# Kernel tuning notes

Hardware: AMD Instinct MI355X
Metric: run time of the kernel (lower is better)

## Reference

```python
import jax, jax.numpy as jnp
import numpy as np

# ---- static problem config (matches init_kwargs / input_specs) ----
L = 8                      # num_labels
D = H = W = 96             # volume dims
N = D * H * W
ALPHA, BETA, GAMMA = 8.0, 0.125, 3.0
NIT = 5                    # num_iterations
# 4-D bilateral grid dims: 3 spatial axes scaled by alpha, 1 intensity axis scaled by beta
GD = (int(np.ceil((D - 1) / ALPHA)) + 2,
      int(np.ceil((H - 1) / ALPHA)) + 2,
      int(np.ceil((W - 1) / ALPHA)) + 2,
      int(np.ceil(1.0 / BETA)) + 2)
GSIZE = int(np.prod(GD))
_STRIDES = np.array([GD[1] * GD[2] * GD[3], GD[2] * GD[3], GD[3], 1], dtype=np.int32)


def spatial_gaussian(Q):
    """Exact separable 3D Gaussian filter with sigma=GAMMA. Q: (L, D, H, W)."""
    r = int(3 * GAMMA)
    t = jnp.arange(-r, r + 1, dtype=Q.dtype)
    k = jnp.exp(-0.5 * (t / GAMMA) ** 2)
    k = k / k.sum()
    x = Q[None]  # (1, L, D, H, W)
    for ax in range(3):
        kspatial = [1, 1, 1]
        kspatial[ax] = 2 * r + 1
        kern = jnp.broadcast_to(k.reshape([1, 1] + kspatial), [L, 1] + kspatial)
        pad = [(r, r) if i == ax else (0, 0) for i in range(3)]
        x = jax.lax.conv_general_dilated(
            x, kern, (1, 1, 1), pad, feature_group_count=L,
            dimension_numbers=('NCDHW', 'OIDHW', 'NCDHW'))
    return x[0]


def splat_coords(img):
    """4-D lattice features per voxel. img: (D, H, W). Returns lo (4,N) int32, frac (4,N)."""
    zz, yy, xx = jnp.meshgrid(jnp.arange(D, dtype=img.dtype),
                              jnp.arange(H, dtype=img.dtype),
                              jnp.arange(W, dtype=img.dtype), indexing='ij')
    feats = jnp.stack([zz.reshape(-1) / ALPHA,
                       yy.reshape(-1) / ALPHA,
                       xx.reshape(-1) / ALPHA,
                       img.reshape(-1) / BETA], axis=0)  # (4, N)
    hi = jnp.asarray(GD, feats.dtype).reshape(4, 1) - 2.0
    lo_f = jnp.clip(jnp.floor(feats), 0.0, hi)
    frac = feats - lo_f
    return lo_f.astype(jnp.int32), frac


def blur1(g, ax):
    """[1,2,1]/4 blur along axis ax (grid-unit Gaussian of the splat-blur-slice)."""
    pad = [(0, 0)] * g.ndim
    pad[ax] = (1, 1)
    gp = jnp.pad(g, pad)
    n = g.shape[ax]
    a = jax.lax.slice_in_dim(gp, 0, n, axis=ax)
    b = jax.lax.slice_in_dim(gp, 1, n + 1, axis=ax)
    c = jax.lax.slice_in_dim(gp, 2, n + 2, axis=ax)
    return 0.25 * a + 0.5 * b + 0.25 * c


def lattice_filter(vals, lo, frac):
    """Splat-blur-slice high-dim Gaussian filter. vals: (C, N) -> (C, N)."""
    C = vals.shape[0]
    grid = jnp.zeros((C, GSIZE), vals.dtype)
    idxs, ws = [], []
    for bits in range(16):  # 16 corners of the 4-D cell (multilinear splat)
        off = np.array([(bits >> d) & 1 for d in range(4)], dtype=np.int32)
        w = jnp.prod(jnp.where(off[:, None] == 1, frac, 1.0 - frac), axis=0)  # (N,)
        idx = jnp.sum((lo + off[:, None]) * _STRIDES[:, None], axis=0)        # (N,)
        idxs.append(idx)
        ws.append(w)
        grid = grid.at[:, idx].add(vals * w[None])
    g = grid.reshape((C,) + GD)
    for ax in range(1, 5):
        g = blur1(g, ax)
    gf = g.reshape(C, GSIZE)
    out = jnp.zeros_like(vals)
    for bits in range(16):  # slice
        out = out + ws[bits][None] * gf[:, idxs[bits]]
    return out


def bilateral_apply(Q, lo, frac):
    """Normalized bilateral filtering of Q (L, D, H, W)."""
    vals = jnp.concatenate([Q.reshape(L, N), jnp.ones((1, N), Q.dtype)], axis=0)
    out = lattice_filter(vals, lo, frac)
    return (out[:L] / (out[L:] + 1e-8)).reshape(L, D, H, W)


def reference(U, image, spatial_ker_weights, bilateral_ker_weights, compatibility_matrix):
    Us = U[0]                               # (L, D, H, W); batch must be 1
    lo, frac = splat_coords(image[0, 0])    # lattice built once from image (as in __init__)
    Q = Us
    for _ in range(NIT):
        # NOTE: original code recomputes softmax of the (unchanged) unary U each iteration
        Qsm = jax.nn.softmax(Us, axis=0)
        sp = spatial_gaussian(Qsm).reshape(L, -1)
        bi = bilateral_apply(Qsm, lo, frac).reshape(L, -1)
        Qp = compatibility_matrix @ (spatial_ker_weights @ sp + bilateral_ker_weights @ bi)
        Q = Us + Qp.reshape(L, D, H, W)
    return jax.nn.softmax(Q, axis=0)[None]


def setup_inputs() -> dict:
    key = jax.random.key(0)
    k1, k2 = jax.random.split(key)
    U = jax.random.normal(k1, (1, L, D, H, W), jnp.float32)
    image = jax.random.uniform(k2, (1, 1, D, H, W), jnp.float32)
    eye = jnp.eye(L, dtype=jnp.float32)
    return {
        "U": U,
        "image": image,
        "spatial_ker_weights": 3.0 * eye,     # spatial_ker_weight * I
        "bilateral_ker_weights": 10.0 * eye,  # bilateral_ker_weight * I
        "compatibility_matrix": eye,
    }
```

## Files before the change

kernel.cpp:

```cpp
#include <hip/hip_runtime.h>
#include <math.h>

#define LBL   8
#define DIM   96
#define PLANE (DIM*DIM)
#define NVOX  (DIM*DIM*DIM)
#define GD0 14
#define GD1 14
#define GD2 14
#define GD3 10
#define GSIZE (GD0*GD1*GD2*GD3)
#define ST0 1960
#define ST1 140
#define ST2 10
#define CH  12
#define NBLK 12
#define NBLKS (NBLK*NBLK*NBLK)
#define PART 720
#define GOUT (GSIZE*9)
#define SUP 513
#define ROW8 (DIM/8)
#define PLANE8 (PLANE/8)
#define VOL8 (NVOX/8)
#define XY_BLOCKS 768
#define BLUR_BLOCKS ((GOUT + 255)/256)
#define GRIDF4 (GSIZE*CH/4)

typedef _Float16 half8 __attribute__((ext_vector_type(8)));

__device__ inline half8 h8zero() {
    half8 v;
    #pragma unroll
    for (int e = 0; e < 8; ++e) v[e] = (_Float16)0.f;
    return v;
}

__constant__ float GW[10] = {
    0.13317604f, 0.12597912f, 0.10663904f, 0.08077540f, 0.05475300f,
    0.03320771f, 0.01802341f, 0.00875346f, 0.00380423f, 0.00147945f
};

__global__ __launch_bounds__(512)
void k_zero(float4* __restrict__ g)
{
    const int i = blockIdx.x*512 + threadIdx.x;
    if (i < GRIDF4) {
        float4 z; z.x = 0.f; z.y = 0.f; z.z = 0.f; z.w = 0.f;
        g[i] = z;
    }
}

__global__ __launch_bounds__(512)
void k_softmax_splat(const float* __restrict__ U, const float* __restrict__ img,
                     _Float16* __restrict__ lnq, float* __restrict__ grid)
{
    __shared__ float sF[512];
    __shared__ __align__(16) unsigned char uball[2880 * 4];
    __shared__ _Float16 sA[64*180];

    _Float16* sU = (_Float16*)uball;
    float*    sB = (float*)uball;

    const int tid = threadIdx.x;
    const int bid0 = blockIdx.x;
    const int bid = (bid0 & 7) * (NBLKS >> 3) + (bid0 >> 3);
    const int bx = bid % NBLK;
    const int by = (bid / NBLK) % NBLK;
    const int bz = bid / (NBLK*NBLK);

    const int lx = tid & 7;
    const int ly = (tid >> 3) & 7;
    const int lz = tid >> 6;

    const int x = bx*8 + lx;
    const int y = by*8 + ly;
    const int z = bz*8 + lz;
    const int vox = z * PLANE + y * DIM + x;

    {
        float t[LBL], e[LBL];
        float m = -1e30f;
        #pragma unroll
        for (int l = 0; l < LBL; ++l) { t[l] = U[l*NVOX + vox]; m = fmaxf(m, t[l]); }
        float ssum = 0.f;
        #pragma unroll
        for (int l = 0; l < LBL; ++l) { t[l] -= m; e[l] = __expf(t[l]); ssum += e[l]; }
        const float inv  = 1.f / ssum;
        const float logs = __logf(ssum);
        #pragma unroll
        for (int l = 0; l < LBL; ++l) {
            lnq[l*NVOX + vox] = (_Float16)(t[l] - logs);
            sU[l*SUP + tid]   = (_Float16)(e[l] * inv);
        }
        sU[8*SUP + tid] = (_Float16)1.0f;
        sF[tid] = img[vox] * 8.0f;
    }
    __syncthreads();

    {
        const int cgrp = tid & 3;
        const int k2   = (tid >> 2) & 1;
        const int row  = tid >> 3;
        const int cb   = cgrp * 2;

        float bins[10][3];
        #pragma unroll
        for (int g = 0; g < 10; ++g) { bins[g][0]=0.f; bins[g][1]=0.f; bins[g][2]=0.f; }

        for (int vx = 0; vx < 8; ++vx) {
            const int vi = row*8 + vx;
            const float f  = sF[vi];
            const float wx = k2 ? (float)vx*0.125f : 1.f - (float)vx*0.125f;
            const float u0 = (float)sU[cb*SUP + vi];
            const float u1 = (float)sU[(cb+1)*SUP + vi];
            const float u2 = (float)sU[8*SUP + vi];
            #pragma unroll
            for (int g = 0; g < 10; ++g) {
                float w = fmaxf(1.f - fabsf(f - (float)g), 0.f) * wx;
                bins[g][0] += w*u0; bins[g][1] += w*u1; bins[g][2] += w*u2;
            }
        }
        _Float16* pA = sA + row*180 + k2*90;
        #pragma unroll
        for (int g = 0; g < 10; ++g) {
            pA[g*9 + cb]     = (_Float16)bins[g][0];
            pA[g*9 + cb + 1] = (_Float16)bins[g][1];
            if (cgrp == 3) pA[g*9 + 8] = (_Float16)bins[g][2];
        }
    }
    __syncthreads();

    if (tid < 288) {
        const int c   = tid % 9;
        const int k2  = (tid / 9) & 1;
        const int j2  = (tid / 18) & 1;
        const int lzo = tid / 36;
        float S[10];
        #pragma unroll
        for (int g = 0; g < 10; ++g) S[g] = 0.f;
        for (int ly2 = 0; ly2 < 8; ++ly2) {
            const float wy = j2 ? (float)ly2*0.125f : 1.f - (float)ly2*0.125f;
            const _Float16* pA = sA + (lzo*8 + ly2)*180 + k2*90;
            #pragma unroll
            for (int g = 0; g < 10; ++g) S[g] += wy * (float)pA[g*9 + c];
        }
        float* pB = sB + lzo*360 + j2*180 + k2*90;
        #pragma unroll
        for (int g = 0; g < 10; ++g) pB[g*9 + c] = S[g];
    }
    __syncthreads();

    for (int item = tid; item < PART; item += 512) {
        const int t  = item / 90;
        const int gc = item % 90;
        const int g  = gc / 9;
        const int c  = gc % 9;
        const int i2 = t >> 2, j2 = (t >> 1) & 1, k2 = t & 1;
        float acc = 0.f;
        #pragma unroll
        for (int lzo = 0; lzo < 8; ++lzo) {
            const float wz = i2 ? (float)lzo*0.125f : 1.f - (float)lzo*0.125f;
            acc += wz * sB[lzo*360 + j2*180 + k2*90 + gc];
        }
        const int cell = (bz + i2)*ST0 + (by + j2)*ST1 + (bx + k2)*ST2 + g;
        atomicAdd(&grid[cell*CH + c], acc);
    }
}

__global__ __launch_bounds__(256)
void k_xy_blur(const half8* __restrict__ lnq, half8* __restrict__ dst,
               const float* __restrict__ gsrc, float* __restrict__ gdst)
{
    __shared__ _Float16 sIn[PLANE];
    __shared__ _Float16 sX[PLANE];

    const int tid = threadIdx.x;

    if (blockIdx.x >= XY_BLOCKS) {
        const int item = (blockIdx.x - XY_BLOCKS)*256 + tid;
        if (item >= GOUT) return;
        const int c    = item % 9;
        const int cell = item / 9;
        const int gz = cell / ST0;
        int r = cell % ST0;
        const int gy = r / ST1;  r %= ST1;
        const int gx = r / ST2;
        const int g  = r % ST2;

        const int crd[4] = {gz, gy, gx, g};
        const int ext[4] = {GD0, GD1, GD2, GD3};
        const int str[4] = {ST0, ST1, ST2, 1};
        float wa[4][3];
        int   oa[4][3];
        #pragma unroll
        for (int ax = 0; ax < 4; ++ax)
            #pragma unroll
            for (int dd = 0; dd < 3; ++dd) {
                const int cc = crd[ax] + dd - 1;
                const bool ok = (cc >= 0 && cc < ext[ax]);
                wa[ax][dd] = ok ? (dd == 1 ? 0.5f : 0.25f) : 0.f;
                oa[ax][dd] = ok ? (dd - 1) * str[ax] : 0;
            }

        float acc = 0.f;
        #pragma unroll
        for (int a = 0; a < 3; ++a) {
            const float w0 = wa[0][a];
            #pragma unroll
            for (int b = 0; b < 3; ++b) {
                const float w1 = w0 * wa[1][b];
                #pragma unroll
                for (int d2 = 0; d2 < 3; ++d2) {
                    const float w2 = w1 * wa[2][d2];
                    const int ob = oa[0][a] + oa[1][b] + oa[2][d2];
                    #pragma unroll
                    for (int e = 0; e < 3; ++e)
                        acc += w2 * wa[3][e] * gsrc[(cell + ob + oa[3][e])*CH + c];
                }
            }
        }
        gdst[cell*CH + c] = acc;
        return;
    }

    half8* sIn8 = (half8*)sIn;
    half8* sX8  = (half8*)sX;
    const size_t base8 = (size_t)blockIdx.x * PLANE8;

    for (int i = tid; i < PLANE8; i += 256) {
        const half8 v = lnq[base8 + i];
        half8 w;
        #pragma unroll
        for (int e = 0; e < 8; ++e) w[e] = (_Float16)__expf((float)v[e]);
        sIn8[i] = w;
    }
    __syncthreads();

    for (int it = tid; it < 576; it += 256) {
        const int seg = it % 6;
        const int row = it / 6;
        float w[48];
        #pragma unroll
        for (int k = 0; k < 6; ++k) {
            const int j8 = 2*seg - 2 + k;
            half8 v = h8zero();
            if (j8 >= 0 && j8 < ROW8) v = sIn8[row*ROW8 + j8];
            #pragma unroll
            for (int e = 0; e < 8; ++e) w[k*8 + e] = (float)v[e];
        }
        half8 o0 = h8zero(), o1 = h8zero();
        #pragma unroll
        for (int i = 0; i < 16; ++i) {
            float acc = 0.f;
            #pragma unroll
            for (int t = -9; t <= 9; ++t) acc += GW[t < 0 ? -t : t] * w[i + 16 + t];
            if (i < 8) o0[i] = (_Float16)acc; else o1[i - 8] = (_Float16)acc;
        }
        sX8[row*ROW8 + 2*seg]     = o0;
        sX8[row*ROW8 + 2*seg + 1] = o1;
    }
    __syncthreads();

    for (int it = tid; it < 288; it += 256) {
        const int x8   = it % ROW8;
        const int yseg = it / ROW8;
        const int ct = yseg * 4;
        float acc[4][8];
        #pragma unroll
        for (int k = 0; k < 4; ++k)
            #pragma unroll
            for (int e = 0; e < 8; ++e) acc[k][e] = 0.f;
        #pragma unroll
        for (int jj = 0; jj < 22; ++jj) {
            const int j = ct - 9 + jj;
            if (j < 0 || j >= DIM) continue;
            const half8 v = sX8[j*ROW8 + x8];
            float f[8];
            #pragma unroll
            for (int e = 0; e < 8; ++e) f[e] = (float)v[e];
            #pragma unroll
            for (int k = 0; k < 4; ++k) {
                const int d = jj - 9 - k;
                if (d >= -9 && d <= 9) {
                    const float wgt = GW[d < 0 ? -d : d];
                    #pragma unroll
                    for (int e = 0; e < 8; ++e) acc[k][e] += wgt * f[e];
                }
            }
        }
        #pragma unroll
        for (int k = 0; k < 4; ++k) {
            half8 o;
            #pragma unroll
            for (int e = 0; e < 8; ++e) o[e] = (_Float16)acc[k][e];
            dst[base8 + (ct + k)*ROW8 + x8] = o;
        }
    }
}

__global__ __launch_bounds__(256)
void k_gauss_z(const half8* __restrict__ src, half8* __restrict__ dst)
{
    const int bid = blockIdx.x;
    const int swz = (bid & 7) * (864 >> 3) + (bid >> 3);
    const int u = swz * 256 + threadIdx.x;

    const int x8 = u % ROW8;
    const int yy = (u / ROW8) % DIM;
    const int ztl = u / (ROW8 * DIM);
    const int zt = ztl % (DIM/4);
    const int l  = ztl / (DIM/4);
    const int base8 = l * VOL8 + yy * ROW8 + x8;
    const int ct = zt * 4;

    float acc[4][8];
    #pragma unroll
    for (int k = 0; k < 4; ++k)
        #pragma unroll
        for (int e = 0; e < 8; ++e) acc[k][e] = 0.f;

    #pragma unroll
    for (int jj = 0; jj < 22; ++jj) {
        const int j = ct - 9 + jj;
        if (j < 0 || j >= DIM) continue;
        const half8 v = src[base8 + j*PLANE8];
        float f[8];
        #pragma unroll
        for (int e = 0; e < 8; ++e) f[e] = (float)v[e];
        #pragma unroll
        for (int k = 0; k < 4; ++k) {
            const int d = jj - 9 - k;
            if (d >= -9 && d <= 9) {
                const float wgt = GW[d < 0 ? -d : d];
                #pragma unroll
                for (int e = 0; e < 8; ++e) acc[k][e] += wgt * f[e];
            }
        }
    }
    #pragma unroll
    for (int k = 0; k < 4; ++k) {
        half8 o;
        #pragma unroll
        for (int e = 0; e < 8; ++e) o[e] = (_Float16)acc[k][e];
        dst[base8 + (ct + k)*PLANE8] = o;
    }
}

__global__ __launch_bounds__(512)
void k_final(const _Float16* __restrict__ lnq, const _Float16* __restrict__ sp,
             const float* __restrict__ grid, const float* __restrict__ img,
             const float* __restrict__ Cm, const float* __restrict__ Sw,
             const float* __restrict__ Bw, float* __restrict__ out)
{
    __shared__ float sm[128];
    __shared__ __align__(16) float sG[1800];

    const int tid = threadIdx.x;
    if (tid < 64) {
        const int i = tid >> 3, j = tid & 7;
        float cs = 0.f, cb = 0.f;
        #pragma unroll
        for (int k = 0; k < 8; ++k) {
            cs += Cm[i*8 + k] * Sw[k*8 + j];
            cb += Cm[i*8 + k] * Bw[k*8 + j];
        }
        sm[tid] = cs;
        sm[64 + tid] = cb;
    }

    const int bid0 = blockIdx.x;
    const int bid = (bid0 & 7) * (1728 >> 3) + (bid0 >> 3);
    const int bxi = bid % 3;
    const int byi = (bid / 3) % 6;
    const int z   = bid / 18;

    const int zc0 = z >> 3;
    const float fz = (float)(z & 7) * 0.125f;

    for (int item = tid; item < 1800; item += 512) {
        const int c    = item % 12;
        const int cell = item / 12;
        const int g  = cell % 10;
        const int xc = (cell / 10) % 5;
        const int yc = cell / 50;
        const int cellA = zc0*ST0 + (byi*2 + yc)*ST1 + (bxi*4 + xc)*ST2 + g;
        sG[item] = (1.f - fz)*grid[cellA*CH + c] + fz*grid[(cellA + ST0)*CH + c];
    }
    __syncthreads();

    const int lx  = tid & 31;
    const int lyt = tid >> 5;
    const int x = bxi*32 + lx;
    const int y = byi*16 + lyt;
    const int vox = z*PLANE + y*DIM + x;

    const float f = img[vox] * 8.0f;
    int li = (int)floorf(f);
    li = li < 0 ? 0 : (li > 8 ? 8 : li);
    const float fi = f - (float)li;
    const float fy = (float)(y & 7) * 0.125f;
    const float fx = (float)(x & 7) * 0.125f;
    const float wyv[2] = {1.f - fy, fy};
    const float wxv[2] = {1.f - fx, fx};
    const float wiv[2] = {1.f - fi, fi};
    const int ycb = lyt >> 3;
    const int xcb = lx >> 3;

    float acc[9];
    #pragma unroll
    for (int c = 0; c < 9; ++c) acc[c] = 0.f;

    #pragma unroll
    for (int j2 = 0; j2 < 2; ++j2)
    #pragma unroll
    for (int k2 = 0; k2 < 2; ++k2) {
        const float wsp = wyv[j2] * wxv[k2];
        const int base = (((ycb + j2)*5 + (xcb + k2))*10 + li)*12;
        #pragma unroll
        for (int m2 = 0; m2 < 2; ++m2) {
            const float w = wsp * wiv[m2];
            const float* p = &sG[base + m2*12];
            const float4 p0 = *reinterpret_cast<const float4*>(p);
            const float4 p1 = *reinterpret_cast<const float4*>(p + 4);
            acc[0] += w * p0.x; acc[1] += w * p0.y; acc[2] += w * p0.z; acc[3] += w * p0.w;
            acc[4] += w * p1.x; acc[5] += w * p1.y; acc[6] += w * p1.z; acc[7] += w * p1.w;
            acc[8] += w * p[8];
        }
    }
    const float dinv = 1.f / (acc[8] + 1e-8f);

    float spv[LBL], lq[LBL];
    #pragma unroll
    for (int l = 0; l < LBL; ++l) {
        spv[l] = (float)sp[(size_t)l*NVOX + vox];
        lq[l]  = (float)lnq[(size_t)l*NVOX + vox];
    }

    float v[LBL];
    float mx = -1e30f;
    #pragma unroll
    for (int i = 0; i < LBL; ++i) {
        float t = 0.f;
        #pragma unroll
        for (int l = 0; l < LBL; ++l)
            t += sm[i*8 + l] * spv[l] + sm[64 + i*8 + l] * (acc[l] * dinv);
        v[i] = lq[i] + t;
        mx = fmaxf(mx, v[i]);
    }
    float ssum = 0.f;
    #pragma unroll
    for (int i = 0; i < LBL; ++i) { v[i] = __expf(v[i] - mx); ssum += v[i]; }
    const float inv = 1.f / ssum;
    #pragma unroll
    for (int i = 0; i < LBL; ++i) out[i*NVOX + vox] = v[i] * inv;
}

extern "C" void kernel_launch(void* const* d_in, const int* in_sizes, int n_in,
                              void* d_out, int out_size, void* d_ws, size_t ws_size,
                              hipStream_t stream)
{
    const float* U   = (const float*)d_in[0];
    const float* img = (const float*)d_in[1];
    const float* Sw  = (const float*)d_in[2];
    const float* Bw  = (const float*)d_in[3];
    const float* Cm  = (const float*)d_in[4];
    float* out = (float*)d_out;

    _Float16* qh  = (_Float16*)d_ws;
    _Float16* g1h = qh + (size_t)LBL * NVOX;
    float* gridA  = (float*)(g1h + (size_t)LBL * NVOX);
    float* gridB  = gridA + (size_t)GSIZE * CH;

    k_zero<<<(GRIDF4 + 511)/512, 512, 0, stream>>>((float4*)gridA);

    k_softmax_splat<<<NBLKS, 512, 0, stream>>>(U, img, qh, gridA);

    k_xy_blur<<<XY_BLOCKS + BLUR_BLOCKS, 256, 0, stream>>>(
        (const half8*)qh, (half8*)g1h, gridA, gridB);

    k_gauss_z<<<864, 256, 0, stream>>>((const half8*)g1h,
                                       (half8*)(gridB + (size_t)GSIZE*CH));

    k_final<<<1728, 512, 0, stream>>>(qh,
                                      (const _Float16*)(gridB + (size_t)GSIZE*CH),
                                      gridB, img, Cm, Sw, Bw, out);
}
```

Measured before the change: 78.39 us.

## Replace splat atomics with per-block partials gathered later, drop zero kernel

The splat kernel now writes each block's 720 partial contributions to a dedicated buffer instead of atomically adding them into the grid. A gather pass, run in spare blocks of the xy-blur launch, sums up to 8 neighbouring block partials per grid cell. The grid blur moves into the z-blur launch, and the grid-zeroing kernel is removed. This cuts atomic contention and one launch, at the cost of an extra partial buffer, a separate output buffer for the z blur, and one more pass over the small grid.

Result: no change. 77.40 us (median of 2 runs) (-1.3%).

```diff
diff --git a/kernel.cpp b/kernel.cpp
--- a/kernel.cpp
+++ b/kernel.cpp
@@ -23,8 +23,8 @@
 #define PLANE8 (PLANE/8)
 #define VOL8 (NVOX/8)
 #define XY_BLOCKS 768
-#define BLUR_BLOCKS ((GOUT + 255)/256)
-#define GRIDF4 (GSIZE*CH/4)
+#define GVB ((GOUT + 255)/256)
+#define Z_BLOCKS 864
 
 typedef _Float16 half8 __attribute__((ext_vector_type(8)));
 
@@ -41,18 +41,8 @@
 };
 
 __global__ __launch_bounds__(512)
-void k_zero(float4* __restrict__ g)
-{
-    const int i = blockIdx.x*512 + threadIdx.x;
-    if (i < GRIDF4) {
-        float4 z; z.x = 0.f; z.y = 0.f; z.z = 0.f; z.w = 0.f;
-        g[i] = z;
-    }
-}
-
-__global__ __launch_bounds__(512)
 void k_softmax_splat(const float* __restrict__ U, const float* __restrict__ img,
-                     _Float16* __restrict__ lnq, float* __restrict__ grid)
+                     _Float16* __restrict__ lnq, float* __restrict__ part)
 {
     __shared__ float sF[512];
     __shared__ __align__(16) unsigned char uball[2880 * 4];
@@ -153,8 +143,6 @@
     for (int item = tid; item < PART; item += 512) {
         const int t  = item / 90;
         const int gc = item % 90;
-        const int g  = gc / 9;
-        const int c  = gc % 9;
         const int i2 = t >> 2, j2 = (t >> 1) & 1, k2 = t & 1;
         float acc = 0.f;
         #pragma unroll
@@ -162,14 +150,13 @@
             const float wz = i2 ? (float)lzo*0.125f : 1.f - (float)lzo*0.125f;
             acc += wz * sB[lzo*360 + j2*180 + k2*90 + gc];
         }
-        const int cell = (bz + i2)*ST0 + (by + j2)*ST1 + (bx + k2)*ST2 + g;
-        atomicAdd(&grid[cell*CH + c], acc);
+        part[(size_t)bid*PART + item] = acc;
     }
 }
 
 __global__ __launch_bounds__(256)
-void k_xy_blur(const half8* __restrict__ lnq, half8* __restrict__ dst,
-               const float* __restrict__ gsrc, float* __restrict__ gdst)
+void k_xy_gather(const half8* __restrict__ lnq, half8* __restrict__ dst,
+                 const float* __restrict__ part, float* __restrict__ grid)
 {
     __shared__ _Float16 sIn[PLANE];
     __shared__ _Float16 sX[PLANE];
@@ -178,6 +165,110 @@
 
     if (blockIdx.x >= XY_BLOCKS) {
         const int item = (blockIdx.x - XY_BLOCKS)*256 + tid;
+        if (item >= GOUT) return;
+        const int c    = item % 9;
+        const int cell = item / 9;
+        const int gz = cell / ST0;
+        int r = cell % ST0;
+        const int gy = r / ST1;  r %= ST1;
+        const int gx = r / ST2;
+        const int g  = r % ST2;
+        float acc = 0.f;
+        #pragma unroll
+        for (int t = 0; t < 8; ++t) {
+            const int i2 = t >> 2, j2 = (t >> 1) & 1, k2 = t & 1;
+            const int bz = gz - i2, by = gy - j2, bx = gx - k2;
+            if ((unsigned)bz < (unsigned)NBLK && (unsigned)by < (unsigned)NBLK &&
+                (unsigned)bx < (unsigned)NBLK)
+                acc += part[(size_t)((bz*NBLK + by)*NBLK + bx)*PART + t*90 + g*9 + c];
+        }
+        grid[cell*CH + c] = acc;
+        return;
+    }
+
+    half8* sIn8 = (half8*)sIn;
+    half8* sX8  = (half8*)sX;
+    const size_t base8 = (size_t)blockIdx.x * PLANE8;
+
+    for (int i = tid; i < PLANE8; i += 256) {
+        const half8 v = lnq[base8 + i];
+        half8 w;
+        #pragma unroll
+        for (int e = 0; e < 8; ++e) w[e] = (_Float16)__expf((float)v[e]);
+        sIn8[i] = w;
+    }
+    __syncthreads();
+
+    for (int it = tid; it < 576; it += 256) {
+        const int seg = it % 6;
+        const int row = it / 6;
+        float w[48];
+        #pragma unroll
+        for (int k = 0; k < 6; ++k) {
+            const int j8 = 2*seg - 2 + k;
+            half8 v = h8zero();
+            if (j8 >= 0 && j8 < ROW8) v = sIn8[row*ROW8 + j8];
+            #pragma unroll
+            for (int e = 0; e < 8; ++e) w[k*8 + e] = (float)v[e];
+        }
+        half8 o0 = h8zero(), o1 = h8zero();
+        #pragma unroll
+        for (int i = 0; i < 16; ++i) {
+            float acc = 0.f;
+            #pragma unroll
+            for (int t = -9; t <= 9; ++t) acc += GW[t < 0 ? -t : t] * w[i + 16 + t];
+            if (i < 8) o0[i] = (_Float16)acc; else o1[i - 8] = (_Float16)acc;
+        }
+        sX8[row*ROW8 + 2*seg]     = o0;
+        sX8[row*ROW8 + 2*seg + 1] = o1;
+    }
+    __syncthreads();
+
+    for (int it = tid; it < 288; it += 256) {
+        const int x8   = it % ROW8;
+        const int yseg = it / ROW8;
+        const int ct = yseg * 4;
+        float acc[4][8];
+        #pragma unroll
+        for (int k = 0; k < 4; ++k)
+            #pragma unroll
+            for (int e = 0; e < 8; ++e) acc[k][e] = 0.f;
+        #pragma unroll
+        for (int jj = 0; jj < 22; ++jj) {
+            const int j = ct - 9 + jj;
+            if (j < 0 || j >= DIM) continue;
+            const half8 v = sX8[j*ROW8 + x8];
+            float f[8];
+            #pragma unroll
+            for (int e = 0; e < 8; ++e) f[e] = (float)v[e];
+            #pragma unroll
+            for (int k = 0; k < 4; ++k) {
+                const int d = jj - 9 - k;
+                if (d >= -9 && d <= 9) {
+                    const float wgt = GW[d < 0 ? -d : d];
+                    #pragma unroll
+                    for (int e = 0; e < 8; ++e) acc[k][e] += wgt * f[e];
+                }
+            }
+        }
+        #pragma unroll
+        for (int k = 0; k < 4; ++k) {
+            half8 o;
+            #pragma unroll
+            for (int e = 0; e < 8; ++e) o[e] = (_Float16)acc[k][e];
+            dst[base8 + (ct + k)*ROW8 + x8] = o;
+        }
+    }
+}
+
+__global__ __launch_bounds__(256)
+void k_z_blur(const half8* __restrict__ src, half8* __restrict__ dst,
+              const float* __restrict__ gsrc, float* __restrict__ gdst)
+{
+    const int tid = threadIdx.x;
+
+    if (blockIdx.x >= Z_BLOCKS) {
+        const int item = (blockIdx.x - Z_BLOCKS)*256 + tid;
         if (item >= GOUT) return;
         const int c    = item % 9;
         const int cell = item / 9;
@@ -223,87 +314,9 @@
         return;
     }
 
-    half8* sIn8 = (half8*)sIn;
-    half8* sX8  = (half8*)sX;
-    const size_t base8 = (size_t)blockIdx.x * PLANE8;
-
-    for (int i = tid; i < PLANE8; i += 256) {
-        const half8 v = lnq[base8 + i];
-        half8 w;
-        #pragma unroll
-        for (int e = 0; e < 8; ++e) w[e] = (_Float16)__expf((float)v[e]);
-        sIn8[i] = w;
-    }
-    __syncthreads();
-
-    for (int it = tid; it < 576; it += 256) {
-        const int seg = it % 6;
-        const int row = it / 6;
-        float w[48];
-        #pragma unroll
-        for (int k = 0; k < 6; ++k) {
-            const int j8 = 2*seg - 2 + k;
-            half8 v = h8zero();
-            if (j8 >= 0 && j8 < ROW8) v = sIn8[row*ROW8 + j8];
-            #pragma unroll
-            for (int e = 0; e < 8; ++e) w[k*8 + e] = (float)v[e];
-        }
-        half8 o0 = h8zero(), o1 = h8zero();
-        #pragma unroll
-        for (int i = 0; i < 16; ++i) {
-            float acc = 0.f;
-            #pragma unroll
-            for (int t = -9; t <= 9; ++t) acc += GW[t < 0 ? -t : t] * w[i + 16 + t];
-            if (i < 8) o0[i] = (_Float16)acc; else o1[i - 8] = (_Float16)acc;
-        }
-        sX8[row*ROW8 + 2*seg]     = o0;
-        sX8[row*ROW8 + 2*seg + 1] = o1;
-    }
-    __syncthreads();
-
-    for (int it = tid; it < 288; it += 256) {
-        const int x8   = it % ROW8;
-        const int yseg = it / ROW8;
-        const int ct = yseg * 4;
-        float acc[4][8];
-        #pragma unroll
-        for (int k = 0; k < 4; ++k)
-            #pragma unroll
-            for (int e = 0; e < 8; ++e) acc[k][e] = 0.f;
-        #pragma unroll
-        for (int jj = 0; jj < 22; ++jj) {
-            const int j = ct - 9 + jj;
-            if (j < 0 || j >= DIM) continue;
-            const half8 v = sX8[j*ROW8 + x8];
-            float f[8];
-            #pragma unroll
-            for (int e = 0; e < 8; ++e) f[e] = (float)v[e];
-            #pragma unroll
-            for (int k = 0; k < 4; ++k) {
-                const int d = jj - 9 - k;
-                if (d >= -9 && d <= 9) {
-                    const float wgt = GW[d < 0 ? -d : d];
-                    #pragma unroll
-                    for (int e = 0; e < 8; ++e) acc[k][e] += wgt * f[e];
-                }
-            }
-        }
-        #pragma unroll
-        for (int k = 0; k < 4; ++k) {
-            half8 o;
-            #pragma unroll
-            for (int e = 0; e < 8; ++e) o[e] = (_Float16)acc[k][e];
-            dst[base8 + (ct + k)*ROW8 + x8] = o;
-        }
-    }
-}
-
-__global__ __launch_bounds__(256)
-void k_gauss_z(const half8* __restrict__ src, half8* __restrict__ dst)
-{
     const int bid = blockIdx.x;
-    const int swz = (bid & 7) * (864 >> 3) + (bid >> 3);
-    const int u = swz * 256 + threadIdx.x;
+    const int swz = (bid & 7) * (Z_BLOCKS >> 3) + (bid >> 3);
+    const int u = swz * 256 + tid;
 
     const int x8 = u % ROW8;
     const int yy = (u / ROW8) % DIM;
@@ -467,21 +480,20 @@
     float* out = (float*)d_out;
 
     _Float16* qh  = (_Float16*)d_ws;
-    _Float16* g1h = qh + (size_t)LBL * NVOX;
-    float* gridA  = (float*)(g1h + (size_t)LBL * NVOX);
+    _Float16* g1h = qh  + (size_t)LBL * NVOX;
+    _Float16* g2h = g1h + (size_t)LBL * NVOX;
+    float* gridA  = (float*)(g2h + (size_t)LBL * NVOX);
     float* gridB  = gridA + (size_t)GSIZE * CH;
-
-    k_zero<<<(GRIDF4 + 511)/512, 512, 0, stream>>>((float4*)gridA);
-
-    k_softmax_splat<<<NBLKS, 512, 0, stream>>>(U, img, qh, gridA);
-
-    k_xy_blur<<<XY_BLOCKS + BLUR_BLOCKS, 256, 0, stream>>>(
-        (const half8*)qh, (half8*)g1h, gridA, gridB);
-
-    k_gauss_z<<<864, 256, 0, stream>>>((const half8*)g1h,
-                                       (half8*)(gridB + (size_t)GSIZE*CH));
-
-    k_final<<<1728, 512, 0, stream>>>(qh,
-                                      (const _Float16*)(gridB + (size_t)GSIZE*CH),
+    float* part   = gridB + (size_t)GSIZE * CH;
+
+    k_softmax_splat<<<NBLKS, 512, 0, stream>>>(U, img, qh, part);
+
+    k_xy_gather<<<XY_BLOCKS + GVB, 256, 0, stream>>>(
+        (const half8*)qh, (half8*)g1h, part, gridA);
+
+    k_z_blur<<<Z_BLOCKS + GVB, 256, 0, stream>>>(
+        (const half8*)g1h, (half8*)g2h, gridA, gridB);
+
+    k_final<<<1728, 512, 0, stream>>>(qh, (const _Float16*)g2h,
                                       gridB, img, Cm, Sw, Bw, out);
 }
```
